# Kernel optimization log

Hardware: AMD Instinct MI355X
Metric: run time of the kernel (lower is better)

Reference implementation:

```python
import jax, jax.numpy as jnp
import numpy as np

B, S_ENC, T_DEC, I, H = 1024, 49, 25, 76, 2048  # S_ENC = source_seq_len - 1


def setup_inputs() -> dict:
    key = jax.random.key(0)
    ks = jax.random.split(key, 6)
    sc = 0.02
    return {
        "encoder_inputs": jax.random.normal(ks[0], (B, S_ENC, I), jnp.float32),
        "decoder_inputs": jax.random.normal(ks[1], (B, T_DEC, I), jnp.float32),
        "W_ih": jax.random.normal(ks[2], (3 * H, I), jnp.float32) * sc,
        "W_hh": jax.random.normal(ks[3], (3 * H, H), jnp.float32) * sc,
        "b_ih": jnp.zeros((3 * H,), jnp.float32),
        "b_hh": jnp.zeros((3 * H,), jnp.float32),
        "fc_w": jax.random.normal(ks[4], (I, H), jnp.float32) * sc,
        "fc_b": jnp.zeros((I,), jnp.float32),
    }


def gru_cell(x, h, W_ih, W_hh, b_ih, b_hh):
    # PyTorch GRUCell: gates stacked [r; z; n] along first axis of weights.
    gi = x @ W_ih.T + b_ih  # [B, 3H]
    gh = h @ W_hh.T + b_hh  # [B, 3H]
    i_r, i_z, i_n = jnp.split(gi, 3, axis=-1)
    h_r, h_z, h_n = jnp.split(gh, 3, axis=-1)
    r = jax.nn.sigmoid(i_r + h_r)
    z = jax.nn.sigmoid(i_z + h_z)
    n = jnp.tanh(i_n + r * h_n)
    return (1.0 - z) * n + z * h


def reference(encoder_inputs, decoder_inputs, W_ih, W_hh, b_ih, b_hh, fc_w, fc_b):
    # Dropout p=0.0 (and eval mode) -> identity; omitted.
    h0 = jnp.zeros((encoder_inputs.shape[0], H), encoder_inputs.dtype)
    enc = jnp.swapaxes(encoder_inputs, 0, 1)  # [S_ENC, B, I]

    def enc_step(h, x):
        return gru_cell(x, h, W_ih, W_hh, b_ih, b_hh), None

    h, _ = jax.lax.scan(enc_step, h0, enc)

    # Sampling-based decoding: only decoder_inputs[:, 0] is consumed; every
    # later step feeds back the previous output. Each step's input is detached.
    prev0 = decoder_inputs[:, 0, :]

    def dec_step(carry, _):
        h, prev = carry
        inp = jax.lax.stop_gradient(prev)  # inp.detach() in the torch code
        h_new = gru_cell(inp, h, W_ih, W_hh, b_ih, b_hh)
        out = inp + h_new @ fc_w.T + fc_b  # residual over fc1 projection
        return (h_new, out), out

    _, outs = jax.lax.scan(dec_step, (h, prev0), None, length=T_DEC)
    return jnp.swapaxes(outs, 0, 1)  # [B, T_DEC, I]
```

## Files before the change

### kernel.cpp

```cpp
#include <hip/hip_runtime.h>
#include <cstdint>
#include <cstddef>

#define DI __device__ __forceinline__

typedef __bf16 bf16x8 __attribute__((ext_vector_type(8)));
typedef float  f32x4  __attribute__((ext_vector_type(4)));
typedef unsigned short ushort_t;

constexpr int BATCH = 1024;
constexpr int HID   = 2048;
constexpr int IN    = 76;
constexpr int SENC  = 49;
constexpr int TDEC  = 25;
constexpr int KX    = 128;
constexpr int KP    = KX + HID;
constexpr int BK    = 64;
constexpr int KTT   = KP / BK;
constexpr int OSTR  = TDEC * IN;

DI unsigned short f2bf(float f) {
  union { float f; unsigned u; } v; v.f = f;
  unsigned u = v.u;
  return (unsigned short)((u + 0x7fffu + ((u >> 16) & 1u)) >> 16);
}

DI f32x4 mfma16(bf16x8 a, bf16x8 b, f32x4 c) {
  return __builtin_amdgcn_mfma_f32_16x16x32_bf16(a, b, c, 0, 0, 0);
}

DI void gload_lds16(const void* g, void* l) {
  __builtin_amdgcn_global_load_lds((const __attribute__((address_space(1))) void*)g,
                                   (__attribute__((address_space(3))) void*)l,
                                   16, 0, 0);
}

DI float sigmoidf_(float x) { return 1.0f / (1.0f + __expf(-x)); }
DI float tanhf_(float x)    { return 1.0f - 2.0f / (1.0f + __expf(2.0f * x)); }


__global__ void pack_W(const float* __restrict__ Wih, const float* __restrict__ Whh,
                       ushort_t* __restrict__ Wp) {
  int idx = blockIdx.x * 256 + threadIdx.x;
  if (idx >= 6144 * KP) return;
  int n = idx / KP;
  int k = idx - n * KP;
  float v = 0.f;
  if (k < IN)        v = Wih[(size_t)n * IN + k];
  else if (k >= KX)  v = Whh[(size_t)n * HID + (k - KX)];
  Wp[idx] = f2bf(v);
}

__global__ void pack_xe(const float* __restrict__ enc, ushort_t* __restrict__ xe) {
  int idx = blockIdx.x * 256 + threadIdx.x;
  if (idx >= SENC * BATCH * KX) return;
  int t = idx >> 17;
  int rem = idx & 131071;
  int b = rem >> 7, k = rem & 127;
  float v = (k < IN) ? enc[(size_t)b * (SENC * IN) + t * IN + k] : 0.f;
  xe[idx] = f2bf(v);
}

__global__ void pack_xd0(const float* __restrict__ dec, ushort_t* __restrict__ xd) {
  int idx = blockIdx.x * 256 + threadIdx.x;
  if (idx >= BATCH * KX) return;
  int b = idx >> 7, k = idx & 127;
  float v = (k < IN) ? dec[(size_t)b * OSTR + k] : 0.f;
  xd[idx] = f2bf(v);
}

__global__ void pack_fc(const float* __restrict__ fcw, ushort_t* __restrict__ Wfc) {
  int idx = blockIdx.x * 256 + threadIdx.x;
  if (idx >= 80 * HID) return;
  int n = idx >> 11, k = idx & 2047;
  float v = (n < IN) ? fcw[(size_t)n * HID + k] : 0.f;
  Wfc[idx] = f2bf(v);
}

__global__ __launch_bounds__(512, 2) void gru_step_kernel(
    const ushort_t* __restrict__ x,
    const ushort_t* __restrict__ hbp,
    const float*    __restrict__ hfp,
    const ushort_t* __restrict__ Wp,
    const float*    __restrict__ b_ih,
    const float*    __restrict__ b_hh,
    float*          __restrict__ hfn,
    ushort_t*       __restrict__ hbn)
{
  __shared__ ushort_t lds[2][(128 + 192) * BK];

  const int tid  = threadIdx.x;
  const int lane = tid & 63;
  const int wid  = tid >> 6;
  const int bid  = blockIdx.x;
  const int n_grp = (bid & 7) + 8 * (bid >> 6);
  const int m_grp = (bid >> 3) & 7;
  const int row0  = m_grp * 128;
  const int col0  = n_grp * 64;
  const int wm = wid >> 1, wn = wid & 1;

  const int srow  = lane >> 3;
  const int swcol = (((lane & 7) ^ (srow & 7)) << 3);

  const f32x4 Z4 = {0.f, 0.f, 0.f, 0.f};
  f32x4 accr[2][2], accz[2][2], accin[2][2], accN[2][2];
  #pragma unroll
  for (int a = 0; a < 2; ++a)
    #pragma unroll
    for (int b = 0; b < 2; ++b) { accr[a][b] = Z4; accz[a][b] = Z4; accin[a][b] = Z4; accN[a][b] = Z4; }

  const int lr  = lane & 15;
  const int bc  = (lane >> 4) * 16;
  const int ksw0 = ((bc)      ^ ((lane & 7) << 4)) >> 1;
  const int ksw1 = ((64 + bc) ^ ((lane & 7) << 4)) >> 1;

  auto stage = [&](int buf, int kt) {
    const ushort_t* asrc; int astr, ak0;
    if (kt < 2) { asrc = x;   astr = KX;  ak0 = kt * BK; }
    else        { asrc = hbp; astr = HID; ak0 = (kt - 2) * BK; }
    ushort_t* Lb = &lds[buf][0];
    #pragma unroll
    for (int c = 0; c < 2; ++c) {
      const int chunk = wid * 2 + c;
      const ushort_t* g = asrc + (size_t)(row0 + chunk * 8 + srow) * astr + ak0 + swcol;
      gload_lds16(g, Lb + chunk * 512);
    }
    const int wk0 = kt * BK;
    #pragma unroll
    for (int c = 0; c < 3; ++c) {
      const int chunk = wid * 3 + c;
      const int brow = chunk * 8 + srow;
      const int gg = brow >> 6, wi = brow & 63;
      const ushort_t* g = Wp + (size_t)(gg * HID + col0 + wi) * KP + wk0 + swcol;
      gload_lds16(g, Lb + 128 * BK + chunk * 512);
    }
  };

  stage(0, 0);

  for (int kt = 0; kt < KTT; ++kt) {
    if (kt + 1 < KTT) {
      stage((kt + 1) & 1, kt + 1);
      asm volatile("s_waitcnt vmcnt(5)" ::: "memory");
    } else {
      asm volatile("s_waitcnt vmcnt(0)" ::: "memory");
    }
    __builtin_amdgcn_s_barrier();

    {
      const ushort_t* Ab = &lds[kt & 1][0];
      const ushort_t* Bb = &lds[kt & 1][128 * BK];
      #pragma unroll
      for (int ks = 0; ks < 2; ++ks) {
        const int ko = ks ? ksw1 : ksw0;
        bf16x8 af[2], bg[3][2];
        #pragma unroll
        for (int fm = 0; fm < 2; ++fm)
          af[fm] = *reinterpret_cast<const bf16x8*>(&Ab[(wm * 32 + fm * 16 + lr) * BK + ko]);
        #pragma unroll
        for (int g = 0; g < 3; ++g)
          #pragma unroll
          for (int fn = 0; fn < 2; ++fn)
            bg[g][fn] = *reinterpret_cast<const bf16x8*>(&Bb[(g * 64 + wn * 32 + fn * 16 + lr) * BK + ko]);
        #pragma unroll
        for (int fm = 0; fm < 2; ++fm)
          #pragma unroll
          for (int fn = 0; fn < 2; ++fn) {
            accr[fm][fn] = mfma16(af[fm], bg[0][fn], accr[fm][fn]);
            accz[fm][fn] = mfma16(af[fm], bg[1][fn], accz[fm][fn]);
            accN[fm][fn] = mfma16(af[fm], bg[2][fn], accN[fm][fn]);
          }
      }
    }
    if (kt == 1) {
      #pragma unroll
      for (int a = 0; a < 2; ++a)
        #pragma unroll
        for (int b = 0; b < 2; ++b) { accin[a][b] = accN[a][b]; accN[a][b] = Z4; }
    }
    __builtin_amdgcn_s_barrier();
  }

  const int lqb = (lane >> 4) * 4;
  #pragma unroll
  for (int fn = 0; fn < 2; ++fn) {
    const int j = col0 + wn * 32 + fn * 16 + lr;
    const float br  = b_ih[j] + b_hh[j];
    const float bz  = b_ih[HID + j] + b_hh[HID + j];
    const float bin = b_ih[2 * HID + j];
    const float bhn = b_hh[2 * HID + j];
    #pragma unroll
    for (int fm = 0; fm < 2; ++fm) {
      #pragma unroll
      for (int q = 0; q < 4; ++q) {
        const int row = row0 + wm * 32 + fm * 16 + lqb + q;
        const size_t off = (size_t)row * HID + j;
        const float hp = hfp[off];
        const float rr = sigmoidf_(accr[fm][fn][q] + br);
        const float zz = sigmoidf_(accz[fm][fn][q] + bz);
        const float nn = tanhf_(accin[fm][fn][q] + bin + rr * (accN[fm][fn][q] + bhn));
        const float hv = (1.0f - zz) * nn + zz * hp;
        hfn[off] = hv;
        hbn[off] = f2bf(hv);
      }
    }
  }
}

__global__ __launch_bounds__(256) void fc_kernel(
    const ushort_t* __restrict__ hb,
    const ushort_t* __restrict__ Wfc,
    const float*    __restrict__ fc_b,
    const float*    __restrict__ prev,
    float*          __restrict__ outp,
    ushort_t*       __restrict__ xd)
{
  __shared__ float red[4][16][80];
  const int tid = threadIdx.x, lane = tid & 63, wid = tid >> 6;
  const int r0 = blockIdx.x * 16;
  const int lr = lane & 15, lk = (lane >> 4) * 8;
  const f32x4 Z4 = {0.f, 0.f, 0.f, 0.f};
  f32x4 acc[5];
  #pragma unroll
  for (int f = 0; f < 5; ++f) acc[f] = Z4;
  const int kbase = wid * 512;
  #pragma unroll
  for (int ks = 0; ks < 16; ++ks) {
    const int k = kbase + ks * 32 + lk;
    bf16x8 a = *reinterpret_cast<const bf16x8*>(&hb[(size_t)(r0 + lr) * HID + k]);
    #pragma unroll
    for (int f = 0; f < 5; ++f) {
      bf16x8 b = *reinterpret_cast<const bf16x8*>(&Wfc[(size_t)(f * 16 + lr) * HID + k]);
      acc[f] = mfma16(a, b, acc[f]);
    }
  }
  #pragma unroll
  for (int f = 0; f < 5; ++f)
    #pragma unroll
    for (int q = 0; q < 4; ++q)
      red[wid][(lane >> 4) * 4 + q][f * 16 + lr] = acc[f][q];
  __syncthreads();

  const int rowi = tid >> 4;
  const int j0   = (tid & 15) * 8;
  const int b_   = r0 + rowi;
  #pragma unroll
  for (int jj = 0; jj < 8; ++jj) {
    const int j = j0 + jj;
    float ov = 0.f;
    if (j < IN) {
      float s = red[0][rowi][j] + red[1][rowi][j] + red[2][rowi][j] + red[3][rowi][j];
      ov = prev[(size_t)b_ * OSTR + j] + fc_b[j] + s;
      outp[(size_t)b_ * OSTR + j] = ov;
    }
    xd[b_ * KX + j] = f2bf(j < IN ? ov : 0.f);
  }
}

extern "C" void kernel_launch(void* const* d_in, const int* in_sizes, int n_in,
                              void* d_out, int out_size, void* d_ws, size_t ws_size,
                              hipStream_t stream) {
  const float* enc = (const float*)d_in[0];
  const float* dec = (const float*)d_in[1];
  const float* Wih = (const float*)d_in[2];
  const float* Whh = (const float*)d_in[3];
  const float* bih = (const float*)d_in[4];
  const float* bhh = (const float*)d_in[5];
  const float* fcw = (const float*)d_in[6];
  const float* fcb = (const float*)d_in[7];
  float* out = (float*)d_out;

  char* ws = (char*)d_ws;
  ushort_t* Wp  = (ushort_t*)ws;  ws += (size_t)6144 * KP * 2;
  ushort_t* xe  = (ushort_t*)ws;  ws += (size_t)SENC * BATCH * KX * 2;
  ushort_t* xd  = (ushort_t*)ws;  ws += (size_t)BATCH * KX * 2;
  ushort_t* Wfc = (ushort_t*)ws;  ws += (size_t)80 * HID * 2;
  float* hf0 = (float*)ws;        ws += (size_t)BATCH * HID * 4;
  float* hf1 = (float*)ws;        ws += (size_t)BATCH * HID * 4;
  ushort_t* hb0 = (ushort_t*)ws;  ws += (size_t)BATCH * HID * 2;
  ushort_t* hb1 = (ushort_t*)ws;  ws += (size_t)BATCH * HID * 2;
  float* hf[2] = {hf0, hf1};
  ushort_t* hbp[2] = {hb0, hb1};

  pack_W  <<<(6144 * KP + 255) / 256, 256, 0, stream>>>(Wih, Whh, Wp);
  pack_xe <<<(SENC * BATCH * KX + 255) / 256, 256, 0, stream>>>(enc, xe);
  pack_xd0<<<(BATCH * KX + 255) / 256, 256, 0, stream>>>(dec, xd);
  pack_fc <<<(80 * HID + 255) / 256, 256, 0, stream>>>(fcw, Wfc);
  hipMemsetAsync(hf0, 0, (size_t)BATCH * HID * 4, stream);
  hipMemsetAsync(hb0, 0, (size_t)BATCH * HID * 2, stream);

  for (int s = 0; s < SENC + TDEC; ++s) {
    const ushort_t* xsrc = (s < SENC) ? (xe + (size_t)s * BATCH * KX) : xd;
    gru_step_kernel<<<256, 512, 0, stream>>>(xsrc, hbp[s & 1], hf[s & 1], Wp, bih, bhh,
                                             hf[(s + 1) & 1], hbp[(s + 1) & 1]);
    if (s >= SENC) {
      const int t = s - SENC;
      const float* prev = (t == 0) ? dec : (out + (size_t)(t - 1) * IN);
      fc_kernel<<<64, 256, 0, stream>>>(hbp[(s + 1) & 1], Wfc, fcb, prev,
                                        out + (size_t)t * IN, xd);
    }
  }
}
```

Measured before the change: 2.789 ms.

## Triple-buffer LDS staging and split each K tile into prioritized MFMA phases

The LDS ring grows from two to three buffers, so global-to-LDS loads run two K tiles ahead instead of one. Each K tile is split into two sub-steps. Each sub-step loads its fragments into registers, waits with explicit lgkmcnt/vmcnt counts and barriers, then issues its MFMAs at raised wave priority, with sched_barriers to fix the order. The aim is to hide global load latency and overlap LDS reads with matrix math. In exchange, each block needs about 120KB of LDS, which can limit how many blocks fit on a CU, and there are more barriers per K tile.

```diff
diff --git a/kernel.cpp b/kernel.cpp
--- a/kernel.cpp
+++ b/kernel.cpp
@@ -87,7 +87,7 @@
     float*          __restrict__ hfn,
     ushort_t*       __restrict__ hbn)
 {
-  __shared__ ushort_t lds[2][(128 + 192) * BK];
+  __shared__ ushort_t lds[3][(128 + 192) * BK];
 
   const int tid  = threadIdx.x;
   const int lane = tid & 63;
@@ -137,48 +137,75 @@
   };
 
   stage(0, 0);
+  stage(1, 1);
+  asm volatile("s_waitcnt vmcnt(5)" ::: "memory");
+  __builtin_amdgcn_s_barrier();
 
   for (int kt = 0; kt < KTT; ++kt) {
-    if (kt + 1 < KTT) {
-      stage((kt + 1) & 1, kt + 1);
-      asm volatile("s_waitcnt vmcnt(5)" ::: "memory");
-    } else {
-      asm volatile("s_waitcnt vmcnt(0)" ::: "memory");
-    }
+    const ushort_t* Ab = &lds[kt % 3][0];
+    const ushort_t* Bb = &lds[kt % 3][128 * BK];
+
+    bf16x8 af0[2], bg0[3][2];
+    #pragma unroll
+    for (int fm = 0; fm < 2; ++fm)
+      af0[fm] = *reinterpret_cast<const bf16x8*>(&Ab[(wm * 32 + fm * 16 + lr) * BK + ksw0]);
+    #pragma unroll
+    for (int g = 0; g < 3; ++g)
+      #pragma unroll
+      for (int fn = 0; fn < 2; ++fn)
+        bg0[g][fn] = *reinterpret_cast<const bf16x8*>(&Bb[(g * 64 + wn * 32 + fn * 16 + lr) * BK + ksw0]);
+    if (kt + 2 < KTT) stage((kt + 2) % 3, kt + 2);
+    __builtin_amdgcn_sched_barrier(0);
     __builtin_amdgcn_s_barrier();
-
-    {
-      const ushort_t* Ab = &lds[kt & 1][0];
-      const ushort_t* Bb = &lds[kt & 1][128 * BK];
-      #pragma unroll
-      for (int ks = 0; ks < 2; ++ks) {
-        const int ko = ks ? ksw1 : ksw0;
-        bf16x8 af[2], bg[3][2];
-        #pragma unroll
-        for (int fm = 0; fm < 2; ++fm)
-          af[fm] = *reinterpret_cast<const bf16x8*>(&Ab[(wm * 32 + fm * 16 + lr) * BK + ko]);
-        #pragma unroll
-        for (int g = 0; g < 3; ++g)
-          #pragma unroll
-          for (int fn = 0; fn < 2; ++fn)
-            bg[g][fn] = *reinterpret_cast<const bf16x8*>(&Bb[(g * 64 + wn * 32 + fn * 16 + lr) * BK + ko]);
-        #pragma unroll
-        for (int fm = 0; fm < 2; ++fm)
-          #pragma unroll
-          for (int fn = 0; fn < 2; ++fn) {
-            accr[fm][fn] = mfma16(af[fm], bg[0][fn], accr[fm][fn]);
-            accz[fm][fn] = mfma16(af[fm], bg[1][fn], accz[fm][fn]);
-            accN[fm][fn] = mfma16(af[fm], bg[2][fn], accN[fm][fn]);
-          }
+    asm volatile("s_waitcnt lgkmcnt(0)" ::: "memory");
+    __builtin_amdgcn_sched_barrier(0);
+    __builtin_amdgcn_s_setprio(1);
+    #pragma unroll
+    for (int fm = 0; fm < 2; ++fm)
+      #pragma unroll
+      for (int fn = 0; fn < 2; ++fn) {
+        accr[fm][fn] = mfma16(af0[fm], bg0[0][fn], accr[fm][fn]);
+        accz[fm][fn] = mfma16(af0[fm], bg0[1][fn], accz[fm][fn]);
+        accN[fm][fn] = mfma16(af0[fm], bg0[2][fn], accN[fm][fn]);
       }
-    }
+    __builtin_amdgcn_s_setprio(0);
+    __builtin_amdgcn_sched_barrier(0);
+    __builtin_amdgcn_s_barrier();
+
+    bf16x8 af1[2], bg1[3][2];
+    #pragma unroll
+    for (int fm = 0; fm < 2; ++fm)
+      af1[fm] = *reinterpret_cast<const bf16x8*>(&Ab[(wm * 32 + fm * 16 + lr) * BK + ksw1]);
+    #pragma unroll
+    for (int g = 0; g < 3; ++g)
+      #pragma unroll
+      for (int fn = 0; fn < 2; ++fn)
+        bg1[g][fn] = *reinterpret_cast<const bf16x8*>(&Bb[(g * 64 + wn * 32 + fn * 16 + lr) * BK + ksw1]);
+    if (kt + 2 < KTT) { asm volatile("s_waitcnt vmcnt(5)" ::: "memory"); }
+    else              { asm volatile("s_waitcnt vmcnt(0)" ::: "memory"); }
+    __builtin_amdgcn_sched_barrier(0);
+    __builtin_amdgcn_s_barrier();
+    asm volatile("s_waitcnt lgkmcnt(0)" ::: "memory");
+    __builtin_amdgcn_sched_barrier(0);
+    __builtin_amdgcn_s_setprio(1);
+    #pragma unroll
+    for (int fm = 0; fm < 2; ++fm)
+      #pragma unroll
+      for (int fn = 0; fn < 2; ++fn) {
+        accr[fm][fn] = mfma16(af1[fm], bg1[0][fn], accr[fm][fn]);
+        accz[fm][fn] = mfma16(af1[fm], bg1[1][fn], accz[fm][fn]);
+        accN[fm][fn] = mfma16(af1[fm], bg1[2][fn], accN[fm][fn]);
+      }
+    __builtin_amdgcn_s_setprio(0);
+    __builtin_amdgcn_sched_barrier(0);
+    __builtin_amdgcn_s_barrier();
+
     if (kt == 1) {
       #pragma unroll
       for (int a = 0; a < 2; ++a)
         #pragma unroll
         for (int b = 0; b < 2; ++b) { accin[a][b] = accN[a][b]; accN[a][b] = Z4; }
     }
-    __builtin_amdgcn_s_barrier();
   }
 
   const int lqb = (lane >> 4) * 4;
```

Result: slower. 3.011 ms (+8.0%).

## Triple-buffer LDS tiles and double-buffer MFMA fragments in GRU step GEMM

Applied to the files above, without the earlier changes.

Restructures the GEMM main loop into a software pipeline. LDS grows from two to three stages, and global prefetch runs two tiles ahead. Operand fragments are ping-ponged in registers so LDS reads for the next half-tile overlap the current MFMA burst, with one barrier per iteration. MFMA bursts are wrapped in s_setprio to favour matrix issue. The larger LDS footprint (about 120KB per block) likely prevents two blocks per CU and raises register pressure, trading occupancy for intra-wave overlap.

```diff
diff --git a/kernel.cpp b/kernel.cpp
--- a/kernel.cpp
+++ b/kernel.cpp
@@ -87,7 +87,7 @@
     float*          __restrict__ hfn,
     ushort_t*       __restrict__ hbn)
 {
-  __shared__ ushort_t lds[2][(128 + 192) * BK];
+  __shared__ ushort_t lds[3][(128 + 192) * BK];
 
   const int tid  = threadIdx.x;
   const int lane = tid & 63;
@@ -136,49 +136,65 @@
     }
   };
 
+  auto readFrags = [&](const ushort_t* base, int ko, bf16x8 af[2], bf16x8 bg[3][2]) {
+    const ushort_t* Ab = base;
+    const ushort_t* Bb = base + 128 * BK;
+    #pragma unroll
+    for (int fm = 0; fm < 2; ++fm)
+      af[fm] = *reinterpret_cast<const bf16x8*>(&Ab[(wm * 32 + fm * 16 + lr) * BK + ko]);
+    #pragma unroll
+    for (int g = 0; g < 3; ++g)
+      #pragma unroll
+      for (int fn = 0; fn < 2; ++fn)
+        bg[g][fn] = *reinterpret_cast<const bf16x8*>(&Bb[(g * 64 + wn * 32 + fn * 16 + lr) * BK + ko]);
+  };
+
+  auto burst = [&](bf16x8 af[2], bf16x8 bg[3][2]) {
+    __builtin_amdgcn_s_setprio(1);
+    #pragma unroll
+    for (int fm = 0; fm < 2; ++fm)
+      #pragma unroll
+      for (int fn = 0; fn < 2; ++fn) {
+        accr[fm][fn] = mfma16(af[fm], bg[0][fn], accr[fm][fn]);
+        accz[fm][fn] = mfma16(af[fm], bg[1][fn], accz[fm][fn]);
+        accN[fm][fn] = mfma16(af[fm], bg[2][fn], accN[fm][fn]);
+      }
+    __builtin_amdgcn_s_setprio(0);
+  };
+
   stage(0, 0);
-
-  for (int kt = 0; kt < KTT; ++kt) {
-    if (kt + 1 < KTT) {
-      stage((kt + 1) & 1, kt + 1);
-      asm volatile("s_waitcnt vmcnt(5)" ::: "memory");
-    } else {
-      asm volatile("s_waitcnt vmcnt(0)" ::: "memory");
-    }
+  stage(1, 1);
+  asm volatile("s_waitcnt vmcnt(5)" ::: "memory");
+  __builtin_amdgcn_s_barrier();
+
+  bf16x8 afA[2], bgA[3][2];
+  bf16x8 afB[2], bgB[3][2];
+  readFrags(&lds[0][0], ksw0, afA, bgA);
+
+  for (int kt = 0; kt < KTT - 1; ++kt) {
+    const ushort_t* cur = &lds[kt % 3][0];
+    readFrags(cur, ksw1, afB, bgB);
+    burst(afA, bgA);
+
+    asm volatile("s_waitcnt vmcnt(0)" ::: "memory");
     __builtin_amdgcn_s_barrier();
-
-    {
-      const ushort_t* Ab = &lds[kt & 1][0];
-      const ushort_t* Bb = &lds[kt & 1][128 * BK];
-      #pragma unroll
-      for (int ks = 0; ks < 2; ++ks) {
-        const int ko = ks ? ksw1 : ksw0;
-        bf16x8 af[2], bg[3][2];
-        #pragma unroll
-        for (int fm = 0; fm < 2; ++fm)
-          af[fm] = *reinterpret_cast<const bf16x8*>(&Ab[(wm * 32 + fm * 16 + lr) * BK + ko]);
-        #pragma unroll
-        for (int g = 0; g < 3; ++g)
-          #pragma unroll
-          for (int fn = 0; fn < 2; ++fn)
-            bg[g][fn] = *reinterpret_cast<const bf16x8*>(&Bb[(g * 64 + wn * 32 + fn * 16 + lr) * BK + ko]);
-        #pragma unroll
-        for (int fm = 0; fm < 2; ++fm)
-          #pragma unroll
-          for (int fn = 0; fn < 2; ++fn) {
-            accr[fm][fn] = mfma16(af[fm], bg[0][fn], accr[fm][fn]);
-            accz[fm][fn] = mfma16(af[fm], bg[1][fn], accz[fm][fn]);
-            accN[fm][fn] = mfma16(af[fm], bg[2][fn], accN[fm][fn]);
-          }
-      }
-    }
+    if (kt + 2 < KTT) stage((kt + 2) % 3, kt + 2);
+
+    readFrags(&lds[(kt + 1) % 3][0], ksw0, afA, bgA);
+    burst(afB, bgB);
+
     if (kt == 1) {
       #pragma unroll
       for (int a = 0; a < 2; ++a)
         #pragma unroll
         for (int b = 0; b < 2; ++b) { accin[a][b] = accN[a][b]; accN[a][b] = Z4; }
     }
-    __builtin_amdgcn_s_barrier();
+  }
+  {
+    const ushort_t* cur = &lds[(KTT - 1) % 3][0];
+    readFrags(cur, ksw1, afB, bgB);
+    burst(afA, bgA);
+    burst(afB, bgB);
   }
 
   const int lqb = (lane >> 4) * 4;
```

Result: faster. 2.733 ms (-2.0%).

## Double K tile, software-pipeline LDS fragment reads, drop fp32 hidden state

Applied to the files above, without the earlier changes.

Doubles the K tile to 128 and restructures the GEMM main loop so fragment reads from LDS are ping-ponged against MFMA bursts, with s_setprio raised around the MFMAs and the swizzle pattern redone for the wider rows. This halves the number of barrier/wait rounds per step. It also removes the fp32 hidden-state copy and takes the previous h from the bf16 buffer, cutting global traffic, at the cost of accumulating bf16 rounding in the recurrent state. LDS use doubles to about 160KB per block, which may limit occupancy to one block per CU.

```diff
diff --git a/kernel.cpp b/kernel.cpp
--- a/kernel.cpp
+++ b/kernel.cpp
@@ -15,7 +15,7 @@
 constexpr int TDEC  = 25;
 constexpr int KX    = 128;
 constexpr int KP    = KX + HID;
-constexpr int BK    = 64;
+constexpr int BK    = 128;
 constexpr int KTT   = KP / BK;
 constexpr int OSTR  = TDEC * IN;
 
@@ -23,6 +23,11 @@
   union { float f; unsigned u; } v; v.f = f;
   unsigned u = v.u;
   return (unsigned short)((u + 0x7fffu + ((u >> 16) & 1u)) >> 16);
+}
+
+DI float bf2f(unsigned short h) {
+  union { unsigned u; float f; } v; v.u = ((unsigned)h) << 16;
+  return v.f;
 }
 
 DI f32x4 mfma16(bf16x8 a, bf16x8 b, f32x4 c) {
@@ -80,11 +85,9 @@
 __global__ __launch_bounds__(512, 2) void gru_step_kernel(
     const ushort_t* __restrict__ x,
     const ushort_t* __restrict__ hbp,
-    const float*    __restrict__ hfp,
     const ushort_t* __restrict__ Wp,
     const float*    __restrict__ b_ih,
     const float*    __restrict__ b_hh,
-    float*          __restrict__ hfn,
     ushort_t*       __restrict__ hbn)
 {
   __shared__ ushort_t lds[2][(128 + 192) * BK];
@@ -99,9 +102,6 @@
   const int col0  = n_grp * 64;
   const int wm = wid >> 1, wn = wid & 1;
 
-  const int srow  = lane >> 3;
-  const int swcol = (((lane & 7) ^ (srow & 7)) << 3);
-
   const f32x4 Z4 = {0.f, 0.f, 0.f, 0.f};
   f32x4 accr[2][2], accz[2][2], accin[2][2], accN[2][2];
   #pragma unroll
@@ -109,82 +109,95 @@
     #pragma unroll
     for (int b = 0; b < 2; ++b) { accr[a][b] = Z4; accz[a][b] = Z4; accin[a][b] = Z4; accN[a][b] = Z4; }
 
-  const int lr  = lane & 15;
-  const int bc  = (lane >> 4) * 16;
-  const int ksw0 = ((bc)      ^ ((lane & 7) << 4)) >> 1;
-  const int ksw1 = ((64 + bc) ^ ((lane & 7) << 4)) >> 1;
+  const int l15 = lane & 15;
+  const int lhi = lane >> 4;
 
   auto stage = [&](int buf, int kt) {
     const ushort_t* asrc; int astr, ak0;
-    if (kt < 2) { asrc = x;   astr = KX;  ak0 = kt * BK; }
-    else        { asrc = hbp; astr = HID; ak0 = (kt - 2) * BK; }
+    if (kt == 0) { asrc = x;   astr = KX;  ak0 = 0; }
+    else         { asrc = hbp; astr = HID; ak0 = (kt - 1) * BK; }
     ushort_t* Lb = &lds[buf][0];
     #pragma unroll
-    for (int c = 0; c < 2; ++c) {
-      const int chunk = wid * 2 + c;
-      const ushort_t* g = asrc + (size_t)(row0 + chunk * 8 + srow) * astr + ak0 + swcol;
+    for (int c = 0; c < 4; ++c) {
+      const int chunk = wid * 4 + c;
+      const int rl = chunk * 4 + lhi;
+      const int swz = ((l15 ^ (((chunk & 3) << 2) + lhi)) << 3);
+      const ushort_t* g = asrc + (size_t)(row0 + rl) * astr + ak0 + swz;
       gload_lds16(g, Lb + chunk * 512);
     }
     const int wk0 = kt * BK;
     #pragma unroll
-    for (int c = 0; c < 3; ++c) {
-      const int chunk = wid * 3 + c;
-      const int brow = chunk * 8 + srow;
+    for (int c = 0; c < 6; ++c) {
+      const int chunk = wid * 6 + c;
+      const int brow = chunk * 4 + lhi;
       const int gg = brow >> 6, wi = brow & 63;
-      const ushort_t* g = Wp + (size_t)(gg * HID + col0 + wi) * KP + wk0 + swcol;
+      const int swz = ((l15 ^ (((chunk & 3) << 2) + lhi)) << 3);
+      const ushort_t* g = Wp + (size_t)(gg * HID + col0 + wi) * KP + wk0 + swz;
       gload_lds16(g, Lb + 128 * BK + chunk * 512);
     }
   };
 
+  auto readFrags = [&](const ushort_t* base, int ks, bf16x8 af[2], bf16x8 bg[3][2]) {
+    const int el = (((ks << 2) + lhi) ^ l15) << 3;
+    #pragma unroll
+    for (int fm = 0; fm < 2; ++fm)
+      af[fm] = *reinterpret_cast<const bf16x8*>(&base[(wm * 32 + fm * 16 + l15) * BK + el]);
+    #pragma unroll
+    for (int g = 0; g < 3; ++g)
+      #pragma unroll
+      for (int fn = 0; fn < 2; ++fn)
+        bg[g][fn] = *reinterpret_cast<const bf16x8*>(
+            &base[128 * BK + (g * 64 + wn * 32 + fn * 16 + l15) * BK + el]);
+  };
+
+  auto burst = [&](bf16x8 af[2], bf16x8 bg[3][2]) {
+    __builtin_amdgcn_s_setprio(1);
+    #pragma unroll
+    for (int fm = 0; fm < 2; ++fm)
+      #pragma unroll
+      for (int fn = 0; fn < 2; ++fn) {
+        accr[fm][fn] = mfma16(af[fm], bg[0][fn], accr[fm][fn]);
+        accz[fm][fn] = mfma16(af[fm], bg[1][fn], accz[fm][fn]);
+        accN[fm][fn] = mfma16(af[fm], bg[2][fn], accN[fm][fn]);
+      }
+    __builtin_amdgcn_s_setprio(0);
+  };
+
+  bf16x8 afA[2], bgA[3][2];
+  bf16x8 afB[2], bgB[3][2];
+
   stage(0, 0);
+  asm volatile("s_waitcnt vmcnt(0)" ::: "memory");
+  __builtin_amdgcn_s_barrier();
+  readFrags(&lds[0][0], 0, afA, bgA);
 
   for (int kt = 0; kt < KTT; ++kt) {
-    if (kt + 1 < KTT) {
-      stage((kt + 1) & 1, kt + 1);
-      asm volatile("s_waitcnt vmcnt(5)" ::: "memory");
-    } else {
-      asm volatile("s_waitcnt vmcnt(0)" ::: "memory");
-    }
-    __builtin_amdgcn_s_barrier();
-
-    {
-      const ushort_t* Ab = &lds[kt & 1][0];
-      const ushort_t* Bb = &lds[kt & 1][128 * BK];
-      #pragma unroll
-      for (int ks = 0; ks < 2; ++ks) {
-        const int ko = ks ? ksw1 : ksw0;
-        bf16x8 af[2], bg[3][2];
-        #pragma unroll
-        for (int fm = 0; fm < 2; ++fm)
-          af[fm] = *reinterpret_cast<const bf16x8*>(&Ab[(wm * 32 + fm * 16 + lr) * BK + ko]);
-        #pragma unroll
-        for (int g = 0; g < 3; ++g)
-          #pragma unroll
-          for (int fn = 0; fn < 2; ++fn)
-            bg[g][fn] = *reinterpret_cast<const bf16x8*>(&Bb[(g * 64 + wn * 32 + fn * 16 + lr) * BK + ko]);
-        #pragma unroll
-        for (int fm = 0; fm < 2; ++fm)
-          #pragma unroll
-          for (int fn = 0; fn < 2; ++fn) {
-            accr[fm][fn] = mfma16(af[fm], bg[0][fn], accr[fm][fn]);
-            accz[fm][fn] = mfma16(af[fm], bg[1][fn], accz[fm][fn]);
-            accN[fm][fn] = mfma16(af[fm], bg[2][fn], accN[fm][fn]);
-          }
-      }
-    }
-    if (kt == 1) {
+    const ushort_t* base = &lds[kt & 1][0];
+    if (kt + 1 < KTT) stage((kt + 1) & 1, kt + 1);
+
+    readFrags(base, 1, afB, bgB);  burst(afA, bgA);
+    readFrags(base, 2, afA, bgA);  burst(afB, bgB);
+    readFrags(base, 3, afB, bgB);  burst(afA, bgA);
+    burst(afB, bgB);
+
+    if (kt == 0) {
       #pragma unroll
       for (int a = 0; a < 2; ++a)
         #pragma unroll
         for (int b = 0; b < 2; ++b) { accin[a][b] = accN[a][b]; accN[a][b] = Z4; }
     }
-    __builtin_amdgcn_s_barrier();
-  }
-
-  const int lqb = (lane >> 4) * 4;
+
+    if (kt + 1 < KTT) {
+      asm volatile("s_waitcnt vmcnt(0)" ::: "memory");
+      __builtin_amdgcn_s_barrier();
+      readFrags(&lds[(kt + 1) & 1][0], 0, afA, bgA);
+    }
+  }
+
+  const int lqb = lhi * 4;
   #pragma unroll
   for (int fn = 0; fn < 2; ++fn) {
-    const int j = col0 + wn * 32 + fn * 16 + lr;
+    const int j = col0 + wn * 32 + fn * 16 + l15;
     const float br  = b_ih[j] + b_hh[j];
     const float bz  = b_ih[HID + j] + b_hh[HID + j];
     const float bin = b_ih[2 * HID + j];
@@ -195,12 +208,11 @@
       for (int q = 0; q < 4; ++q) {
         const int row = row0 + wm * 32 + fm * 16 + lqb + q;
         const size_t off = (size_t)row * HID + j;
-        const float hp = hfp[off];
+        const float hp = bf2f(hbp[off]);
         const float rr = sigmoidf_(accr[fm][fn][q] + br);
         const float zz = sigmoidf_(accz[fm][fn][q] + bz);
         const float nn = tanhf_(accin[fm][fn][q] + bin + rr * (accN[fm][fn][q] + bhn));
         const float hv = (1.0f - zz) * nn + zz * hp;
-        hfn[off] = hv;
         hbn[off] = f2bf(hv);
       }
     }
@@ -275,24 +287,20 @@
   ushort_t* xe  = (ushort_t*)ws;  ws += (size_t)SENC * BATCH * KX * 2;
   ushort_t* xd  = (ushort_t*)ws;  ws += (size_t)BATCH * KX * 2;
   ushort_t* Wfc = (ushort_t*)ws;  ws += (size_t)80 * HID * 2;
-  float* hf0 = (float*)ws;        ws += (size_t)BATCH * HID * 4;
-  float* hf1 = (float*)ws;        ws += (size_t)BATCH * HID * 4;
   ushort_t* hb0 = (ushort_t*)ws;  ws += (size_t)BATCH * HID * 2;
   ushort_t* hb1 = (ushort_t*)ws;  ws += (size_t)BATCH * HID * 2;
-  float* hf[2] = {hf0, hf1};
   ushort_t* hbp[2] = {hb0, hb1};
 
   pack_W  <<<(6144 * KP + 255) / 256, 256, 0, stream>>>(Wih, Whh, Wp);
   pack_xe <<<(SENC * BATCH * KX + 255) / 256, 256, 0, stream>>>(enc, xe);
   pack_xd0<<<(BATCH * KX + 255) / 256, 256, 0, stream>>>(dec, xd);
   pack_fc <<<(80 * HID + 255) / 256, 256, 0, stream>>>(fcw, Wfc);
-  hipMemsetAsync(hf0, 0, (size_t)BATCH * HID * 4, stream);
   hipMemsetAsync(hb0, 0, (size_t)BATCH * HID * 2, stream);
 
   for (int s = 0; s < SENC + TDEC; ++s) {
     const ushort_t* xsrc = (s < SENC) ? (xe + (size_t)s * BATCH * KX) : xd;
-    gru_step_kernel<<<256, 512, 0, stream>>>(xsrc, hbp[s & 1], hf[s & 1], Wp, bih, bhh,
-                                             hf[(s + 1) & 1], hbp[(s + 1) & 1]);
+    gru_step_kernel<<<256, 512, 0, stream>>>(xsrc, hbp[s & 1], Wp, bih, bhh,
+                                             hbp[(s + 1) & 1]);
     if (s >= SENC) {
       const int t = s - SENC;
       const float* prev = (t == 0) ? dec : (out + (size_t)(t - 1) * IN);
```

After: 2.631 ms. 5.7% less time.
